# Kernel optimization log

Measured on AMD Instinct MI355X. Metric: run time of the kernel, lower is better.

Reference implementation:

```python
import jax, jax.numpy as jnp
import numpy as np

B, N, DIN, D, HID, C, K = 16, 1024, 768, 512, 128, 20, 64
H = W = 32
EPS = 1e-5  # BatchNorm eps (inference mode with running stats)


def _conv(x, w, pad=0, dil=1):
    return jax.lax.conv_general_dilated(
        x, w, (1, 1), [(pad, pad), (pad, pad)],
        rhs_dilation=(dil, dil),
        dimension_numbers=('NCHW', 'OIHW', 'NCHW'))


def _bn(x, g, b, m, v):
    inv = jax.lax.rsqrt(v + EPS)
    return (x - m[None, :, None, None]) * (g * inv)[None, :, None, None] + b[None, :, None, None]


def _l2norm(x):
    n = jnp.sqrt(jnp.sum(x * x, axis=-1, keepdims=True))
    return x / jnp.maximum(n, 1e-12)  # matches F.normalize(eps=1e-12)


def setup_inputs():
    key = jax.random.key(0)
    ks = jax.random.split(key, 12)

    def conv_w(k, o, i, kh, kw):
        return jax.random.normal(k, (o, i, kh, kw), jnp.float32) / np.sqrt(i * kh * kw)

    def bn_p(k, c):
        k1, k2 = jax.random.split(k)
        return (jnp.ones(c, jnp.float32), jnp.zeros(c, jnp.float32),
                0.1 * jax.random.normal(k1, (c,), jnp.float32),
                jax.random.uniform(k2, (c,), jnp.float32, 0.5, 1.5))

    g0, b0, m0, v0 = bn_p(ks[3], D)
    gr, br, mr, vr = bn_p(ks[4], HID)
    gl, bl, ml, vl = bn_p(ks[5], HID)
    gg, bg, mg, vg = bn_p(ks[6], HID)
    gp, bp, mp, vp = bn_p(ks[7], D)
    return {
        'patch_feats': jax.random.normal(ks[0], (B, N, DIN), jnp.float32),
        'protos': _l2norm(jax.random.normal(ks[1], (C, K, D), jnp.float32)),  # hybrid protos, L2-normed as in __init__
        'w0': conv_w(ks[2], D, DIN, 1, 1), 'g0': g0, 'b0': b0, 'm0': m0, 'v0': v0,
        'wr': conv_w(ks[8], HID, D, 1, 1), 'gr': gr, 'br': br, 'mr': mr, 'vr': vr,
        'wl': conv_w(ks[9], HID, HID, 3, 3), 'gl': gl, 'bl': bl, 'ml': ml, 'vl': vl,
        'wg': conv_w(ks[10], HID, HID, 3, 3), 'gg': gg, 'bg': bg, 'mg': mg, 'vg': vg,
        'wp': conv_w(ks[11], D, 2 * HID, 1, 1), 'gp': gp, 'bp': bp, 'mp': mp, 'vp': vp,
        'wf': conv_w(jax.random.fold_in(key, 99), D, D, 1, 1),
        'bf': jnp.zeros(D, jnp.float32),
        'logit_scale': jnp.float32(10.0),
    }


def reference(patch_feats, protos, w0, g0, b0, m0, v0, wr, gr, br, mr, vr,
              wl, gl, bl, ml, vl, wg, gg, bg, mg, vg, wp, gp, bp, mp, vp,
              wf, bf, logit_scale):
    Bq, Nq, Din = patch_feats.shape
    x = patch_feats.transpose(0, 2, 1).reshape(Bq, Din, H, W)
    # adapter: 1x1 conv -> BN -> ReLU
    x = jax.nn.relu(_bn(_conv(x, w0), g0, b0, m0, v0))
    # ResidualContextBlock
    res = x
    o = jax.nn.relu(_bn(_conv(x, wr), gr, br, mr, vr))
    l = jax.nn.relu(_bn(_conv(o, wl, pad=1), gl, bl, ml, vl))
    g = jax.nn.relu(_bn(_conv(o, wg, pad=2, dil=2), gg, bg, mg, vg))
    o = _bn(_conv(jnp.concatenate([l, g], axis=1), wp), gp, bp, mp, vp)
    x = jax.nn.relu(o + res)
    # final 1x1 conv (with bias)
    x = _conv(x, wf) + bf[None, :, None, None]
    # back to [B, N, D], L2 normalize
    x = x.reshape(Bq, D, Nq).transpose(0, 2, 1)
    x = _l2norm(x)
    # per-class cosine sims + double max reduction (vectorized over classes)
    sims = jnp.einsum('bnd,ckd->bcnk', x, protos)  # [B,C,N,K]
    A = sims.max(axis=-1)                          # [B,C,N] patch->proto max
    act_maps = A.reshape(Bq, C, H, W)
    logits = A.max(axis=-1) * logit_scale          # [B,C]
    return logits, act_maps, x
```

## Files before the change

kernel.cpp:

```cpp
#include <hip/hip_runtime.h>
#include <math.h>

#define BN_EPS 1e-5f

typedef __attribute__((ext_vector_type(8))) short short8v;
typedef __attribute__((ext_vector_type(8))) unsigned short ushort8v;
typedef __attribute__((ext_vector_type(4))) float f32x4;

__device__ __forceinline__ unsigned short f2b(float f) {
    unsigned int u = __float_as_uint(f);
    return (unsigned short)((u + 0x7FFFu + ((u >> 16) & 1u)) >> 16);
}
__device__ __forceinline__ float b2f(unsigned short h) {
    return __uint_as_float(((unsigned int)h) << 16);
}

typedef __attribute__((address_space(1))) const unsigned int gas_uint;
typedef __attribute__((address_space(3))) unsigned int las_uint;
__device__ __forceinline__ void gload16(const void* g, void* l) {
    __builtin_amdgcn_global_load_lds((gas_uint*)g, (las_uint*)l, 16, 0, 0);
}

#define VMCNT2()  asm volatile("s_waitcnt vmcnt(2)"  ::: "memory")
#define VMCNT3()  asm volatile("s_waitcnt vmcnt(3)"  ::: "memory")
#define VMCNT4()  asm volatile("s_waitcnt vmcnt(4)"  ::: "memory")
#define VMCNT6()  asm volatile("s_waitcnt vmcnt(6)"  ::: "memory")
#define VMCNT0()  asm volatile("s_waitcnt vmcnt(0)"  ::: "memory")
#define LGKM0()   asm volatile("s_waitcnt lgkmcnt(0)" ::: "memory")
#define SBAR()    __builtin_amdgcn_s_barrier()
#define SCHED0()  __builtin_amdgcn_sched_barrier(0)

__global__ __launch_bounds__(256) void prep_all(
    const float* __restrict__ w0,  const float* __restrict__ wr,
    const float* __restrict__ wp,  const float* __restrict__ wf,
    const float* __restrict__ prot,
    const float* __restrict__ wl,  const float* __restrict__ wg,
    unsigned short* __restrict__ w0_o, unsigned short* __restrict__ wr_o,
    unsigned short* __restrict__ wp_o, unsigned short* __restrict__ wf_o,
    unsigned short* __restrict__ prot_o,
    unsigned short* __restrict__ wt_o, unsigned short* __restrict__ opad)
{
    int i = blockIdx.x * 256 + threadIdx.x;
    if (i >= 557056) return;
    if (i >= 225280) {
        ushort8v z;
#pragma unroll
        for (int k = 0; k < 8; ++k) z[k] = 0;
        *(ushort8v*)(opad + (size_t)(i - 225280) * 8) = z;
        return;
    }
    if (i >= 188416) {
        int e0 = (i - 188416) * 8;
        ushort8v u;
#pragma unroll
        for (int q = 0; q < 8; ++q) {
            int e = e0 + q;
            int br = e >= 147456;
            int j  = e - br * 147456;
            int tap = j >> 14, oc = (j >> 7) & 127, ic = j & 127;
            const float* src = br ? wg : wl;
            u[q] = f2b(src[((oc << 7) + ic) * 9 + tap]);
        }
        *(ushort8v*)(wt_o + (size_t)e0) = u;
        return;
    }
    const float* src; unsigned short* dst; int off;
    if      (i <  49152) { src = w0;   dst = w0_o;   off = i; }
    else if (i <  57344) { src = wr;   dst = wr_o;   off = i - 49152; }
    else if (i <  73728) { src = wp;   dst = wp_o;   off = i - 57344; }
    else if (i < 106496) { src = wf;   dst = wf_o;   off = i - 73728; }
    else                 { src = prot; dst = prot_o; off = i - 106496; }
    const float4* p = (const float4*)(src + (size_t)off * 8);
    float4 a = p[0], b = p[1];
    ushort8v r;
    r[0] = f2b(a.x); r[1] = f2b(a.y); r[2] = f2b(a.z); r[3] = f2b(a.w);
    r[4] = f2b(b.x); r[5] = f2b(b.y); r[6] = f2b(b.z); r[7] = f2b(b.w);
    *(ushort8v*)(dst + (size_t)off * 8) = r;
}

__global__ __launch_bounds__(256, 3) void mfma_gemm_f32a(
    const float* __restrict__ A, int lda,
    const unsigned short* __restrict__ Wt, int ldw,
    unsigned short* __restrict__ outp, int ldc, int Kdim,
    const float* __restrict__ bng, const float* __restrict__ bnb,
    const float* __restrict__ bnm, const float* __restrict__ bnv)
{
    __shared__ short8v Asta[2][512];
    __shared__ short8v Bsta[2][512];
    const int t  = threadIdx.x;
    const int l  = t & 63, wv = t >> 6;
    const int wm = wv >> 1, wn = wv & 1;
    const int m0 = blockIdx.x << 7, n0 = blockIdx.y << 7;

    const int r0  = t & 127;
    const int kb0 = t >> 7;

    const float*          Apf = A  + (size_t)(m0 + r0) * lda + kb0 * 8;
    const unsigned short* Bp  = Wt + (size_t)(n0 + r0) * ldw + kb0 * 8;

    f32x4 acc[4][4];
#pragma unroll
    for (int mf = 0; mf < 4; ++mf)
#pragma unroll
        for (int nf = 0; nf < 4; ++nf)
#pragma unroll
            for (int j = 0; j < 4; ++j) acc[mf][nf][j] = 0.f;

    const int arow = wm * 64 + (l & 15);
    const int brow = wn * 64 + (l & 15);
    const int kq   = l >> 4;
    const int nK   = Kdim >> 5;

    float4 areg[2][2];

#define LOADA(k0)                                                   \
    do {                                                            \
        areg[0][0] = *(const float4*)(Apf + (k0));                  \
        areg[0][1] = *(const float4*)(Apf + (k0) + 4);              \
        areg[1][0] = *(const float4*)(Apf + (k0) + 16);             \
        areg[1][1] = *(const float4*)(Apf + (k0) + 20);             \
    } while (0)

#define WRITEA(buf)                                                 \
    do {                                                            \
        _Pragma("unroll")                                           \
        for (int c_ = 0; c_ < 2; ++c_) {                            \
            ushort8v u_;                                            \
            u_[0] = f2b(areg[c_][0].x); u_[1] = f2b(areg[c_][0].y); \
            u_[2] = f2b(areg[c_][0].z); u_[3] = f2b(areg[c_][0].w); \
            u_[4] = f2b(areg[c_][1].x); u_[5] = f2b(areg[c_][1].y); \
            u_[6] = f2b(areg[c_][1].z); u_[7] = f2b(areg[c_][1].w); \
            *(ushort8v*)&Asta[buf][t + 256 * c_] = u_;              \
        }                                                           \
    } while (0)

#define STAGEB(buf, k0)                                      \
    do {                                                     \
        gload16(Bp + (k0),      &Bsta[buf][wv * 64]);        \
        gload16(Bp + (k0) + 16, &Bsta[buf][wv * 64 + 256]);  \
    } while (0)

    LOADA(0);
    STAGEB(0, 0);
    VMCNT2();
    WRITEA(0);
    VMCNT0(); LGKM0();
    SBAR();

    int cur = 0;
    for (int ks = 0; ks < nK; ++ks) {
        const bool more = (ks + 1 < nK);
        if (more) {
            LOADA((ks + 1) << 5);
            STAGEB(cur ^ 1, (ks + 1) << 5);
        }
        short8v af[4], bfv[4];
#pragma unroll
        for (int mf = 0; mf < 4; ++mf) af[mf]  = Asta[cur][kq * 128 + arow + mf * 16];
#pragma unroll
        for (int nf = 0; nf < 4; ++nf) bfv[nf] = Bsta[cur][kq * 128 + brow + nf * 16];
#pragma unroll
        for (int mf = 0; mf < 4; ++mf)
#pragma unroll
            for (int nf = 0; nf < 4; ++nf)
                acc[mf][nf] = __builtin_amdgcn_mfma_f32_16x16x32_bf16(
                    af[mf], bfv[nf], acc[mf][nf], 0, 0, 0);
        if (more) {
            VMCNT2();
            WRITEA(cur ^ 1);
        }
        LGKM0(); SCHED0();
        VMCNT0();
        SBAR();
        cur ^= 1;
    }
#undef LOADA
#undef WRITEA
#undef STAGEB

    float s[4], sh[4];
    int cols[4];
#pragma unroll
    for (int nf = 0; nf < 4; ++nf) {
        int col = n0 + wn * 64 + nf * 16 + (l & 15);
        cols[nf] = col;
        float sc = bng[col] * rsqrtf(bnv[col] + BN_EPS);
        s[nf]  = sc;
        sh[nf] = bnb[col] - bnm[col] * sc;
    }
#pragma unroll
    for (int mf = 0; mf < 4; ++mf) {
#pragma unroll
        for (int j = 0; j < 4; ++j) {
            int row = m0 + wm * 64 + mf * 16 + kq * 4 + j;
#pragma unroll
            for (int nf = 0; nf < 4; ++nf) {
                float v = fmaxf(acc[mf][nf][j] * s[nf] + sh[nf], 0.f);
                outp[(size_t)row * ldc + cols[nf]] = f2b(v);
            }
        }
    }
}

template <int EPI>
__global__ __launch_bounds__(256, 3) void mfma_gemm(
    const unsigned short* __restrict__ A, int lda,
    const unsigned short* __restrict__ Wt, int ldw,
    void* __restrict__ outp, int ldc, int Kdim,
    const float* __restrict__ bng, const float* __restrict__ bnb,
    const float* __restrict__ bnm, const float* __restrict__ bnv,
    const unsigned short* __restrict__ res, int ldres,
    const float* __restrict__ bias)
{
    __shared__ short8v Asta[2][512];
    __shared__ short8v Bsta[2][512];
    const int t  = threadIdx.x;
    const int l  = t & 63, wv = t >> 6;
    const int wm = wv >> 1, wn = wv & 1;
    const int m0 = blockIdx.x << 7, n0 = blockIdx.y << 7;

    const int r0  = t & 127;
    const int kb0 = t >> 7;

    const unsigned short* Ap = A  + (size_t)(m0 + r0) * lda + kb0 * 8;
    const unsigned short* Bp = Wt + (size_t)(n0 + r0) * ldw + kb0 * 8;

    f32x4 acc[4][4];
#pragma unroll
    for (int mf = 0; mf < 4; ++mf)
#pragma unroll
        for (int nf = 0; nf < 4; ++nf)
#pragma unroll
            for (int j = 0; j < 4; ++j) acc[mf][nf][j] = 0.f;

    const int arow = wm * 64 + (l & 15);
    const int brow = wn * 64 + (l & 15);
    const int kq   = l >> 4;
    const int nK   = Kdim >> 5;

#define STAGE_G(buf, k0)                                     \
    do {                                                     \
        gload16(Ap + (k0),      &Asta[buf][wv * 64]);        \
        gload16(Ap + (k0) + 16, &Asta[buf][wv * 64 + 256]);  \
        gload16(Bp + (k0),      &Bsta[buf][wv * 64]);        \
        gload16(Bp + (k0) + 16, &Bsta[buf][wv * 64 + 256]);  \
    } while (0)

    STAGE_G(0, 0);
    int cur = 0;
    for (int ks = 0; ks < nK; ++ks) {
        if (ks + 1 < nK) { STAGE_G(cur ^ 1, (ks + 1) << 5); VMCNT4(); }
        else             { VMCNT0(); }
        SBAR();
        short8v af[4], bfv[4];
#pragma unroll
        for (int mf = 0; mf < 4; ++mf) af[mf]  = Asta[cur][kq * 128 + arow + mf * 16];
#pragma unroll
        for (int nf = 0; nf < 4; ++nf) bfv[nf] = Bsta[cur][kq * 128 + brow + nf * 16];
#pragma unroll
        for (int mf = 0; mf < 4; ++mf)
#pragma unroll
            for (int nf = 0; nf < 4; ++nf)
                acc[mf][nf] = __builtin_amdgcn_mfma_f32_16x16x32_bf16(
                    af[mf], bfv[nf], acc[mf][nf], 0, 0, 0);
        LGKM0(); SCHED0();
        SBAR();
        cur ^= 1;
    }
#undef STAGE_G

    float s[4], sh[4];
    int cols[4];
#pragma unroll
    for (int nf = 0; nf < 4; ++nf) {
        int col = n0 + wn * 64 + nf * 16 + (l & 15);
        cols[nf] = col;
        if (EPI == 2) { s[nf] = 1.f; sh[nf] = bias[col]; }
        else {
            float sc = bng[col] * rsqrtf(bnv[col] + BN_EPS);
            s[nf]  = sc;
            sh[nf] = bnb[col] - bnm[col] * sc;
        }
    }
#pragma unroll
    for (int mf = 0; mf < 4; ++mf) {
#pragma unroll
        for (int j = 0; j < 4; ++j) {
            int row = m0 + wm * 64 + mf * 16 + kq * 4 + j;
#pragma unroll
            for (int nf = 0; nf < 4; ++nf) {
                float v = acc[mf][nf][j] * s[nf] + sh[nf];
                if (EPI == 1) v += b2f(res[(size_t)row * ldres + cols[nf]]);
                if (EPI != 2) v = fmaxf(v, 0.f);
                if (EPI == 2) {
                    ((float*)outp)[(size_t)row * ldc + cols[nf]] = v;
                } else {
                    ((unsigned short*)outp)[(size_t)row * ldc + cols[nf]] = f2b(v);
                }
            }
        }
    }
}

__global__ __launch_bounds__(256, 3) void mfma_gemm64_pad(
    const unsigned short* __restrict__ A,
    const unsigned short* __restrict__ Wt,
    unsigned short* __restrict__ opad,
    const float* __restrict__ bng, const float* __restrict__ bnb,
    const float* __restrict__ bnm, const float* __restrict__ bnv)
{
    __shared__ short8v Asta[2][256];
    __shared__ short8v Bsta[2][512];
    const int t  = threadIdx.x;
    const int l  = t & 63, wv = t >> 6;
    const int wm = wv >> 1, wn = wv & 1;
    const int m0 = blockIdx.x << 6;

    const unsigned short* Ap = A  + (size_t)(m0 + (t & 63)) * 512 + (t >> 6) * 8;
    const unsigned short* Bp = Wt + (size_t)(t & 127) * 512 + (t >> 7) * 8;

    f32x4 acc[2][4];
#pragma unroll
    for (int mf = 0; mf < 2; ++mf)
#pragma unroll
        for (int nf = 0; nf < 4; ++nf)
#pragma unroll
            for (int j = 0; j < 4; ++j) acc[mf][nf][j] = 0.f;

    const int arow = wm * 32 + (l & 15);
    const int brow = wn * 64 + (l & 15);
    const int kq   = l >> 4;

#define STAGE_R(buf, k0)                                     \
    do {                                                     \
        gload16(Ap + (k0),      &Asta[buf][wv * 64]);        \
        gload16(Bp + (k0),      &Bsta[buf][wv * 64]);        \
        gload16(Bp + (k0) + 16, &Bsta[buf][wv * 64 + 256]);  \
    } while (0)

    STAGE_R(0, 0);
    int cur = 0;
    for (int ks = 0; ks < 16; ++ks) {
        if (ks + 1 < 16) { STAGE_R(cur ^ 1, (ks + 1) << 5); VMCNT3(); }
        else             { VMCNT0(); }
        SBAR();
        short8v af[2], bfv[4];
#pragma unroll
        for (int mf = 0; mf < 2; ++mf) af[mf]  = Asta[cur][kq * 64 + arow + mf * 16];
#pragma unroll
        for (int nf = 0; nf < 4; ++nf) bfv[nf] = Bsta[cur][kq * 128 + brow + nf * 16];
#pragma unroll
        for (int mf = 0; mf < 2; ++mf)
#pragma unroll
            for (int nf = 0; nf < 4; ++nf)
                acc[mf][nf] = __builtin_amdgcn_mfma_f32_16x16x32_bf16(
                    af[mf], bfv[nf], acc[mf][nf], 0, 0, 0);
        LGKM0(); SCHED0();
        SBAR();
        cur ^= 1;
    }
#undef STAGE_R

    float s[4], sh[4];
    int cols[4];
#pragma unroll
    for (int nf = 0; nf < 4; ++nf) {
        int col = wn * 64 + nf * 16 + (l & 15);
        cols[nf] = col;
        float sc = bng[col] * rsqrtf(bnv[col] + BN_EPS);
        s[nf]  = sc;
        sh[nf] = bnb[col] - bnm[col] * sc;
    }
#pragma unroll
    for (int mf = 0; mf < 2; ++mf) {
#pragma unroll
        for (int j = 0; j < 4; ++j) {
            int row = m0 + wm * 32 + mf * 16 + kq * 4 + j;
            int b = row >> 10, h = (row >> 5) & 31, ww = row & 31;
            size_t pbase = ((size_t)(b * 36 + h + 2) * 36 + (ww + 2)) * 128;
#pragma unroll
            for (int nf = 0; nf < 4; ++nf) {
                float v = fmaxf(acc[mf][nf][j] * s[nf] + sh[nf], 0.f);
                opad[pbase + cols[nf]] = f2b(v);
            }
        }
    }
}

__global__ __launch_bounds__(256, 3) void conv_mfma(
    const unsigned short* __restrict__ opad,
    const unsigned short* __restrict__ wt_all,
    const float* __restrict__ g1, const float* __restrict__ b1,
    const float* __restrict__ m1, const float* __restrict__ v1,
    const float* __restrict__ g2, const float* __restrict__ b2,
    const float* __restrict__ m2, const float* __restrict__ v2,
    unsigned short* __restrict__ lg)
{
    __shared__ short8v Asta[2][512];
    __shared__ short8v Bsta[2][1024];
    const int t = threadIdx.x;
    const int l = t & 63, wv = t >> 6;
    const int wm = wv >> 1, wn = wv & 1;
    const int m0 = blockIdx.x << 6;
    const int br = blockIdx.y;
    const int dil = 1 + br;
    const unsigned short* wtb = wt_all + (size_t)br * 147456;

    const int r0 = t & 63;
    const int m  = m0 + r0;
    const int bb = m >> 10, h = (m >> 5) & 31, wc = m & 31;
    const ptrdiff_t pbase = ((ptrdiff_t)(bb * 36 + h + 2) * 36 + (wc + 2)) * 128;
    const unsigned short* ApT = opad + pbase + (t >> 6) * 8;
    const unsigned short* BpT = wtb + (size_t)(t & 127) * 128 + (t >> 7) * 8;

    f32x4 acc[2][4];
#pragma unroll
    for (int mf = 0; mf < 2; ++mf)
#pragma unroll
        for (int nf = 0; nf < 4; ++nf)
#pragma unroll
            for (int j = 0; j < 4; ++j) acc[mf][nf][j] = 0.f;

    const int arow = wm * 32 + (l & 15);
    const int bcol = wn * 64 + (l & 15);
    const int kq   = l >> 4;

#define STAGE_C(buf, s)                                                        \
    do {                                                                       \
        int tap_ = (s) >> 1, hh_ = ((s) & 1) * 64;                             \
        int dh_ = tap_ / 3 - 1, dw_ = tap_ % 3 - 1;                            \
        const unsigned short* Ap_ = ApT + (ptrdiff_t)((dh_ * 36 + dw_) * dil) * 128 + hh_; \
        const unsigned short* Bp_ = BpT + (size_t)tap_ * 16384 + hh_;          \
        gload16(Ap_,      &Asta[buf][wv * 64]);                                \
        gload16(Ap_ + 32, &Asta[buf][wv * 64 + 256]);                          \
        gload16(Bp_,      &Bsta[buf][wv * 64]);                                \
        gload16(Bp_ + 16, &Bsta[buf][wv * 64 + 256]);                          \
        gload16(Bp_ + 32, &Bsta[buf][wv * 64 + 512]);                          \
        gload16(Bp_ + 48, &Bsta[buf][wv * 64 + 768]);                          \
    } while (0)

    STAGE_C(0, 0);
    int cur = 0;
    for (int s = 0; s < 18; ++s) {
        if (s + 1 < 18) { STAGE_C(cur ^ 1, s + 1); VMCNT6(); }
        else            { VMCNT0(); }
        SBAR();
        short8v af[2][2], bfv[2][4];
#pragma unroll
        for (int kk = 0; kk < 2; ++kk) {
            int kb = kk * 4 + kq;
            af[kk][0] = Asta[cur][kb * 64 + arow];
            af[kk][1] = Asta[cur][kb * 64 + arow + 16];
#pragma unroll
            for (int nf = 0; nf < 4; ++nf)
                bfv[kk][nf] = Bsta[cur][kb * 128 + bcol + nf * 16];
        }
#pragma unroll
        for (int kk = 0; kk < 2; ++kk)
#pragma unroll
            for (int mf = 0; mf < 2; ++mf)
#pragma unroll
                for (int nf = 0; nf < 4; ++nf)
                    acc[mf][nf] = __builtin_amdgcn_mfma_f32_16x16x32_bf16(
                        af[kk][mf], bfv[kk][nf], acc[mf][nf], 0, 0, 0);
        LGKM0(); SCHED0();
        SBAR();
        cur ^= 1;
    }
#undef STAGE_C

    const float* gg = br ? g2 : g1;
    const float* gb = br ? b2 : b1;
    const float* gm = br ? m2 : m1;
    const float* gv = br ? v2 : v1;
    float s4[4], sh[4];
    int cols[4];
#pragma unroll
    for (int nf = 0; nf < 4; ++nf) {
        int col = bcol + nf * 16;
        cols[nf] = col;
        float sc = gg[col] * rsqrtf(gv[col] + BN_EPS);
        s4[nf] = sc;
        sh[nf] = gb[col] - gm[col] * sc;
    }
#pragma unroll
    for (int mf = 0; mf < 2; ++mf) {
#pragma unroll
        for (int j = 0; j < 4; ++j) {
            int row = m0 + wm * 32 + mf * 16 + kq * 4 + j;
#pragma unroll
            for (int nf = 0; nf < 4; ++nf) {
                float v = fmaxf(acc[mf][nf][j] * s4[nf] + sh[nf], 0.f);
                lg[(size_t)row * 256 + br * 128 + cols[nf]] = f2b(v);
            }
        }
    }
}

__global__ __launch_bounds__(256) void l2norm_rows(
    float* __restrict__ x, unsigned short* __restrict__ xn)
{
    const int t    = threadIdx.x;
    const int wv   = t >> 6, lane = t & 63;
    const int row  = (blockIdx.x << 2) + wv;
    float* p = x + (size_t)row * 512 + (lane << 3);
    float4 a = *(float4*)p;
    float4 b = *(float4*)(p + 4);
    float ss = a.x * a.x + a.y * a.y + a.z * a.z + a.w * a.w +
               b.x * b.x + b.y * b.y + b.z * b.z + b.w * b.w;
#pragma unroll
    for (int off = 32; off >= 1; off >>= 1) ss += __shfl_xor(ss, off);
    float sc = 1.f / fmaxf(sqrtf(ss), 1e-12f);
    a.x *= sc; a.y *= sc; a.z *= sc; a.w *= sc;
    b.x *= sc; b.y *= sc; b.z *= sc; b.w *= sc;
    *(float4*)p       = a;
    *(float4*)(p + 4) = b;
    ushort8v r;
    r[0] = f2b(a.x); r[1] = f2b(a.y); r[2] = f2b(a.z); r[3] = f2b(a.w);
    r[4] = f2b(b.x); r[5] = f2b(b.y); r[6] = f2b(b.z); r[7] = f2b(b.w);
    *(ushort8v*)(xn + (size_t)row * 512 + (lane << 3)) = r;
}

__global__ __launch_bounds__(256, 3) void sims_mfma(
    const unsigned short* __restrict__ xn,
    const unsigned short* __restrict__ protos,
    float* __restrict__ act)
{
    __shared__ short8v Asta[2][512];
    __shared__ short8v Bsta[2][512];
    const int t = threadIdx.x;
    const int l = t & 63, wv = t >> 6;
    const int wm = wv >> 1, wn = wv & 1;
    const int m0 = blockIdx.x << 7;

    const int r0  = t & 127, kb0 = t >> 7;
    const unsigned short* Ap = xn + (size_t)(m0 + r0) * 512 + kb0 * 8;
    const unsigned short* Bp = protos + ((size_t)blockIdx.y * 128 + r0) * 512 + kb0 * 8;

    f32x4 acc[4][4];
#pragma unroll
    for (int mf = 0; mf < 4; ++mf)
#pragma unroll
        for (int nf = 0; nf < 4; ++nf)
#pragma unroll
            for (int j = 0; j < 4; ++j) acc[mf][nf][j] = 0.f;

    const int arow = wm * 64 + (l & 15);
    const int brow = wn * 64 + (l & 15);
    const int kq   = l >> 4;

#define STAGE_S(buf, k0)                                     \
    do {                                                     \
        gload16(Ap + (k0),      &Asta[buf][wv * 64]);        \
        gload16(Ap + (k0) + 16, &Asta[buf][wv * 64 + 256]);  \
        gload16(Bp + (k0),      &Bsta[buf][wv * 64]);        \
        gload16(Bp + (k0) + 16, &Bsta[buf][wv * 64 + 256]);  \
    } while (0)

    STAGE_S(0, 0);
    __syncthreads();
    int cur = 0;
    for (int ks = 0; ks < 16; ++ks) {
        short8v af[4], bfv[4];
#pragma unroll
        for (int mf = 0; mf < 4; ++mf) af[mf]  = Asta[cur][kq * 128 + arow + mf * 16];
#pragma unroll
        for (int nf = 0; nf < 4; ++nf) bfv[nf] = Bsta[cur][kq * 128 + brow + nf * 16];
        if (ks + 1 < 16) STAGE_S(cur ^ 1, (ks + 1) << 5);
#pragma unroll
        for (int mf = 0; mf < 4; ++mf)
#pragma unroll
            for (int nf = 0; nf < 4; ++nf)
                acc[mf][nf] = __builtin_amdgcn_mfma_f32_16x16x32_bf16(
                    af[mf], bfv[nf], acc[mf][nf], 0, 0, 0);
        __syncthreads();
        cur ^= 1;
    }
#undef STAGE_S

    const int c = (blockIdx.y << 1) + wn;
#pragma unroll
    for (int mf = 0; mf < 4; ++mf) {
        float vj[4];
#pragma unroll
        for (int j = 0; j < 4; ++j) {
            float v = fmaxf(fmaxf(acc[mf][0][j], acc[mf][1][j]),
                            fmaxf(acc[mf][2][j], acc[mf][3][j]));
            v = fmaxf(v, __shfl_xor(v, 1));
            v = fmaxf(v, __shfl_xor(v, 2));
            v = fmaxf(v, __shfl_xor(v, 4));
            v = fmaxf(v, __shfl_xor(v, 8));
            vj[j] = v;
        }
        if ((l & 15) == 0) {
            int rowb = m0 + wm * 64 + mf * 16 + kq * 4;
#pragma unroll
            for (int j = 0; j < 4; ++j) {
                int row = rowb + j;
                int bb = row >> 10, n = row & 1023;
                act[(((size_t)(bb * 20 + c)) << 10) + n] = vj[j];
            }
        }
    }
}

__global__ __launch_bounds__(256) void logits_max(
    const float* __restrict__ act, const float* __restrict__ lsc,
    float* __restrict__ logits)
{
    const int bc = blockIdx.x;
    const int t  = threadIdx.x;
    float4 v = *(const float4*)(act + ((size_t)bc << 10) + (t << 2));
    float mx = fmaxf(fmaxf(v.x, v.y), fmaxf(v.z, v.w));
#pragma unroll
    for (int off = 32; off >= 1; off >>= 1) mx = fmaxf(mx, __shfl_xor(mx, off));
    __shared__ float wmred[4];
    if ((t & 63) == 0) wmred[t >> 6] = mx;
    __syncthreads();
    if (t == 0) {
        float m2 = fmaxf(fmaxf(wmred[0], wmred[1]), fmaxf(wmred[2], wmred[3]));
        logits[bc] = m2 * lsc[0];
    }
}

extern "C" void kernel_launch(void* const* d_in, const int* in_sizes, int n_in,
                              void* d_out, int out_size, void* d_ws, size_t ws_size,
                              hipStream_t stream)
{
    const float* pf   = (const float*)d_in[0];
    const float* prot = (const float*)d_in[1];
    const float* w0   = (const float*)d_in[2];
    const float* g0   = (const float*)d_in[3];
    const float* b0   = (const float*)d_in[4];
    const float* m0v  = (const float*)d_in[5];
    const float* v0   = (const float*)d_in[6];
    const float* wr   = (const float*)d_in[7];
    const float* gr   = (const float*)d_in[8];
    const float* br   = (const float*)d_in[9];
    const float* mr   = (const float*)d_in[10];
    const float* vr   = (const float*)d_in[11];
    const float* wl   = (const float*)d_in[12];
    const float* gl   = (const float*)d_in[13];
    const float* bl   = (const float*)d_in[14];
    const float* ml   = (const float*)d_in[15];
    const float* vl   = (const float*)d_in[16];
    const float* wg   = (const float*)d_in[17];
    const float* gG   = (const float*)d_in[18];
    const float* bG   = (const float*)d_in[19];
    const float* mG   = (const float*)d_in[20];
    const float* vG   = (const float*)d_in[21];
    const float* wp   = (const float*)d_in[22];
    const float* gp   = (const float*)d_in[23];
    const float* bp   = (const float*)d_in[24];
    const float* mp   = (const float*)d_in[25];
    const float* vp   = (const float*)d_in[26];
    const float* wf   = (const float*)d_in[27];
    const float* bf_  = (const float*)d_in[28];
    const float* lsc  = (const float*)d_in[29];

    char* ws = (char*)d_ws;
    unsigned short* w0_bf    = (unsigned short*)(ws);
    unsigned short* wr_bf    = (unsigned short*)(ws + 786432);
    unsigned short* wt_bf    = (unsigned short*)(ws + 917504);
    unsigned short* wp_bf    = (unsigned short*)(ws + 1507328);
    unsigned short* wf_bf    = (unsigned short*)(ws + 1769472);
    unsigned short* prot_bf  = (unsigned short*)(ws + 2293760);
    unsigned short* x1_bf    = (unsigned short*)(ws + 3604480);
    unsigned short* opad     = (unsigned short*)(ws + 20381696);
    unsigned short* lg_bf    = (unsigned short*)(ws + 25690112);
    unsigned short* x2_bf    = (unsigned short*)(ws + 34078720);
    unsigned short* xn_bf    = (unsigned short*)(ws + 50855936);

    float* out    = (float*)d_out;
    float* logits = out;
    float* act    = out + 320;
    float* xo     = out + 328000;

    prep_all<<<2176, 256, 0, stream>>>(
        w0, wr, wp, wf, prot, wl, wg,
        w0_bf, wr_bf, wp_bf, wf_bf, prot_bf, wt_bf, opad);

    mfma_gemm_f32a<<<dim3(128, 4), 256, 0, stream>>>(
        pf, 768, w0_bf, 768, x1_bf, 512, 768, g0, b0, m0v, v0);

    mfma_gemm64_pad<<<256, 256, 0, stream>>>(
        x1_bf, wr_bf, opad, gr, br, mr, vr);

    conv_mfma<<<dim3(256, 2), 256, 0, stream>>>(
        opad, wt_bf, gl, bl, ml, vl, gG, bG, mG, vG, lg_bf);

    mfma_gemm<1><<<dim3(128, 4), 256, 0, stream>>>(
        lg_bf, 256, wp_bf, 256, x2_bf, 512, 256,
        gp, bp, mp, vp, x1_bf, 512, nullptr);

    mfma_gemm<2><<<dim3(128, 4), 256, 0, stream>>>(
        x2_bf, 512, wf_bf, 512, xo, 512, 512,
        nullptr, nullptr, nullptr, nullptr, nullptr, 0, bf_);

    l2norm_rows<<<4096, 256, 0, stream>>>(xo, xn_bf);

    sims_mfma<<<dim3(128, 10), 256, 0, stream>>>(xn_bf, prot_bf, act);

    logits_max<<<320, 256, 0, stream>>>(act, lsc, logits);
}
```

Before: 189.4 us.

## Deepen first GEMM pipeline to prefetch two K-steps ahead

Restructures the fp32-A MFMA GEMM main loop to issue global loads two K-iterations ahead, using two A register sets and a triple-buffered B LDS stage. The waits are relaxed to partial vmcnt values, so MFMA work overlaps more outstanding memory traffic. This costs extra VGPRs and LDS, which may reduce occupancy under launch_bounds(256,3). The loop is unrolled by two, which assumes nK is even.

```diff
diff --git a/kernel.cpp b/kernel.cpp
--- a/kernel.cpp
+++ b/kernel.cpp
@@ -25,6 +25,7 @@
 #define VMCNT3()  asm volatile("s_waitcnt vmcnt(3)"  ::: "memory")
 #define VMCNT4()  asm volatile("s_waitcnt vmcnt(4)"  ::: "memory")
 #define VMCNT6()  asm volatile("s_waitcnt vmcnt(6)"  ::: "memory")
+#define VMCNT8()  asm volatile("s_waitcnt vmcnt(8)"  ::: "memory")
 #define VMCNT0()  asm volatile("s_waitcnt vmcnt(0)"  ::: "memory")
 #define LGKM0()   asm volatile("s_waitcnt lgkmcnt(0)" ::: "memory")
 #define SBAR()    __builtin_amdgcn_s_barrier()
@@ -86,7 +87,7 @@
     const float* __restrict__ bnm, const float* __restrict__ bnv)
 {
     __shared__ short8v Asta[2][512];
-    __shared__ short8v Bsta[2][512];
+    __shared__ short8v Bsta[3][512];
     const int t  = threadIdx.x;
     const int l  = t & 63, wv = t >> 6;
     const int wm = wv >> 1, wn = wv & 1;
@@ -111,25 +112,25 @@
     const int kq   = l >> 4;
     const int nK   = Kdim >> 5;
 
-    float4 areg[2][2];
-
-#define LOADA(k0)                                                   \
-    do {                                                            \
-        areg[0][0] = *(const float4*)(Apf + (k0));                  \
-        areg[0][1] = *(const float4*)(Apf + (k0) + 4);              \
-        areg[1][0] = *(const float4*)(Apf + (k0) + 16);             \
-        areg[1][1] = *(const float4*)(Apf + (k0) + 20);             \
-    } while (0)
-
-#define WRITEA(buf)                                                 \
+    float4 arA[2][2], arB[2][2];
+
+#define LOADA(AR, k0)                                     \
+    do {                                                  \
+        AR[0][0] = *(const float4*)(Apf + (k0));          \
+        AR[0][1] = *(const float4*)(Apf + (k0) + 4);      \
+        AR[1][0] = *(const float4*)(Apf + (k0) + 16);     \
+        AR[1][1] = *(const float4*)(Apf + (k0) + 20);     \
+    } while (0)
+
+#define WRITEA(AR, buf)                                             \
     do {                                                            \
         _Pragma("unroll")                                           \
         for (int c_ = 0; c_ < 2; ++c_) {                            \
             ushort8v u_;                                            \
-            u_[0] = f2b(areg[c_][0].x); u_[1] = f2b(areg[c_][0].y); \
-            u_[2] = f2b(areg[c_][0].z); u_[3] = f2b(areg[c_][0].w); \
-            u_[4] = f2b(areg[c_][1].x); u_[5] = f2b(areg[c_][1].y); \
-            u_[6] = f2b(areg[c_][1].z); u_[7] = f2b(areg[c_][1].w); \
+            u_[0] = f2b(AR[c_][0].x); u_[1] = f2b(AR[c_][0].y);     \
+            u_[2] = f2b(AR[c_][0].z); u_[3] = f2b(AR[c_][0].w);     \
+            u_[4] = f2b(AR[c_][1].x); u_[5] = f2b(AR[c_][1].y);     \
+            u_[6] = f2b(AR[c_][1].z); u_[7] = f2b(AR[c_][1].w);     \
             *(ushort8v*)&Asta[buf][t + 256 * c_] = u_;              \
         }                                                           \
     } while (0)
@@ -140,43 +141,60 @@
         gload16(Bp + (k0) + 16, &Bsta[buf][wv * 64 + 256]);  \
     } while (0)
 
-    LOADA(0);
+#define MFMA_STEP(ks)                                                          \
+    do {                                                                       \
+        const int cA_ = (ks) & 1;                                              \
+        short8v af_[4], bfv_[4];                                               \
+        _Pragma("unroll")                                                      \
+        for (int mf = 0; mf < 4; ++mf)                                         \
+            af_[mf]  = Asta[cA_][kq * 128 + arow + mf * 16];                   \
+        _Pragma("unroll")                                                      \
+        for (int nf = 0; nf < 4; ++nf)                                         \
+            bfv_[nf] = Bsta[(ks) % 3][kq * 128 + brow + nf * 16];              \
+        _Pragma("unroll")                                                      \
+        for (int mf = 0; mf < 4; ++mf)                                         \
+            _Pragma("unroll")                                                  \
+            for (int nf = 0; nf < 4; ++nf)                                     \
+                acc[mf][nf] = __builtin_amdgcn_mfma_f32_16x16x32_bf16(         \
+                    af_[mf], bfv_[nf], acc[mf][nf], 0, 0, 0);                  \
+    } while (0)
+
+#define STEP(ks, CUR, NXT)                                                     \
+    do {                                                                       \
+        const bool i2_ = (ks) + 2 < nK;                                        \
+        const bool w1_ = (ks) + 1 < nK;                                        \
+        if (i2_) { LOADA(NXT, ((ks) + 2) << 5); STAGEB(((ks) + 2) % 3, ((ks) + 2) << 5); } \
+        if (w1_) {                                                             \
+            if (i2_) VMCNT8(); else VMCNT2();              \
+            WRITEA(CUR, ((ks) + 1) & 1);                                       \
+        }                                                                      \
+        MFMA_STEP(ks);                                                         \
+        if (w1_) {                                                             \
+            if (i2_) VMCNT6(); else VMCNT0();              \
+            LGKM0(); SCHED0();                                                 \
+            SBAR();                                                            \
+        }                                                                      \
+    } while (0)
+
+    LOADA(arA, 0);
     STAGEB(0, 0);
-    VMCNT2();
-    WRITEA(0);
-    VMCNT0(); LGKM0();
+    LOADA(arB, 32);
+    STAGEB(1, 32);
+    VMCNT8();
+    WRITEA(arA, 0);
+    VMCNT6();
+    LGKM0();
     SBAR();
 
-    int cur = 0;
-    for (int ks = 0; ks < nK; ++ks) {
-        const bool more = (ks + 1 < nK);
-        if (more) {
-            LOADA((ks + 1) << 5);
-            STAGEB(cur ^ 1, (ks + 1) << 5);
-        }
-        short8v af[4], bfv[4];
-#pragma unroll
-        for (int mf = 0; mf < 4; ++mf) af[mf]  = Asta[cur][kq * 128 + arow + mf * 16];
-#pragma unroll
-        for (int nf = 0; nf < 4; ++nf) bfv[nf] = Bsta[cur][kq * 128 + brow + nf * 16];
-#pragma unroll
-        for (int mf = 0; mf < 4; ++mf)
-#pragma unroll
-            for (int nf = 0; nf < 4; ++nf)
-                acc[mf][nf] = __builtin_amdgcn_mfma_f32_16x16x32_bf16(
-                    af[mf], bfv[nf], acc[mf][nf], 0, 0, 0);
-        if (more) {
-            VMCNT2();
-            WRITEA(cur ^ 1);
-        }
-        LGKM0(); SCHED0();
-        VMCNT0();
-        SBAR();
-        cur ^= 1;
+    for (int ks = 0; ks < nK; ks += 2) {
+        STEP(ks, arB, arA);
+        STEP(ks + 1, arA, arB);
     }
 #undef LOADA
 #undef WRITEA
 #undef STAGEB
+#undef MFMA_STEP
+#undef STEP
 
     float s[4], sh[4];
     int cols[4];
```

Measured after the change: 191.2 us. About the same (+0.9%).
